# Kernel tuning notes

Hardware: AMD Instinct MI355X
Metric: run time of the kernel (lower is better)

## Reference

```python
import jax, jax.numpy as jnp
import numpy as np

B, S, D, H = 2, 2048, 2048, 16
HD = D // H  # 128
MAX_POS = 2048


def make_sinusoidal_positions(num_pos, dim):
    inv_freq = 1.0 / 10000 ** (np.arange(0, dim, 2) / dim)
    freqs = np.einsum('i,j->ij', np.arange(num_pos), inv_freq).astype('float32')
    emb = np.concatenate((freqs, freqs), axis=-1)  # (num_pos, dim)
    out = np.concatenate((np.sin(emb)[:, None, :], np.cos(emb)[:, None, :]), axis=-1)  # (num_pos,1,2*dim)
    return jnp.array(out[:, :, :num_pos])  # slice is a no-op since num_pos >= 2*dim


_SINCOS = make_sinusoidal_positions(MAX_POS, HD)


def rotate_half(x):
    return jnp.concatenate((-x[..., x.shape[-1] // 2:], x[..., :x.shape[-1] // 2]), axis=-1)


def setup_inputs() -> dict:
    key = jax.random.key(0)
    ks = jax.random.split(key, 5)
    std = 0.02
    return {
        'hidden_states': jax.random.normal(ks[0], (B, S, D), jnp.float32),
        'attention_mask': jnp.ones((B, S), jnp.int32),
        'position_ids': jnp.broadcast_to(jnp.arange(S, dtype=jnp.int32), (B, S)),
        'Wq': jax.random.normal(ks[1], (D, D), jnp.float32) * std,
        'Wk': jax.random.normal(ks[2], (D, D), jnp.float32) * std,
        'Wv': jax.random.normal(ks[3], (D, D), jnp.float32) * std,
        'Wo': jax.random.normal(ks[4], (D, D), jnp.float32) * std,
    }


def reference(hidden_states, attention_mask, position_ids, Wq, Wk, Wv, Wo):
    b, s, d = hidden_states.shape
    # QKV projections, split heads -> (b, s, H, HD)
    q = (hidden_states @ Wq).reshape(b, s, H, HD)
    k = (hidden_states @ Wk).reshape(b, s, H, HD)
    v = (hidden_states @ Wv).reshape(b, s, H, HD)
    # RoPE: embed_positions[position_ids] -> (b, s, 1, 2*HD); split -> sin, cos (b,s,1,HD)
    sincos = _SINCOS[position_ids]
    sin_pos, cos_pos = jnp.split(sincos, 2, axis=-1)
    q = q * cos_pos + rotate_half(q) * sin_pos
    k = k * cos_pos + rotate_half(k) * sin_pos
    # causal + padding mask -> additive bias
    causal = jnp.tril(jnp.ones((s, s), dtype=bool))  # (q, k)
    mask = (attention_mask[:, None, None, :] > 0) & causal[None, None, :, :]  # (b,1,s,s)
    bias = jnp.where(mask, jnp.float32(0.0), jnp.finfo(q.dtype).min).astype(q.dtype)
    # dot_product_attention_weights: scale query, scores + bias, softmax
    scale = jnp.asarray(1.0 / np.sqrt(HD), q.dtype)
    scores = jnp.einsum('bqhd,bkhd->bhqk', q * scale, k) + bias
    attn = jax.nn.softmax(scores, axis=-1)
    out = jnp.einsum('bhqk,bkhd->bqhd', attn, v).reshape(b, s, d)
    return out @ Wo
```

## Files before the change

kernel.cpp:

```cpp
#include <hip/hip_runtime.h>
#include <stdint.h>
#include <math.h>

#define BATCH 2
#define SEQ 2048
#define DM 2048
#define NH 16
#define HD 128

typedef unsigned short u16;
typedef __attribute__((ext_vector_type(8))) __bf16 bf16x8;
typedef __attribute__((ext_vector_type(8))) _Float16 f16x8;
typedef __attribute__((ext_vector_type(4))) float f32x4;
typedef __attribute__((ext_vector_type(4))) unsigned short u16x4;

__device__ inline float bf2f(u16 x) {
    return __uint_as_float(((unsigned)x) << 16);
}
__device__ inline u16 f2bf(float f) {
    unsigned u = __float_as_uint(f);
    return (u16)((u + 0x7FFF + ((u >> 16) & 1)) >> 16);
}
__device__ inline u16 f2h(float f) {
    union { _Float16 h; u16 u; } c;
    c.h = (_Float16)f;
    return c.u;
}
__device__ inline f32x4 mfma16(bf16x8 a, bf16x8 b, f32x4 c) {
    return __builtin_amdgcn_mfma_f32_16x16x32_bf16(a, b, c, 0, 0, 0);
}
__device__ inline f32x4 mfma16h(f16x8 a, f16x8 b, f32x4 c) {
    return __builtin_amdgcn_mfma_f32_16x16x32_f16(a, b, c, 0, 0, 0);
}
__device__ inline void cp16(const u16* g, u16* l) {
    __builtin_amdgcn_global_load_lds(
        (const __attribute__((address_space(1))) unsigned int*)g,
        (__attribute__((address_space(3))) unsigned int*)l, 16, 0, 0);
}

__global__ __launch_bounds__(256) void transpose4(const float* __restrict__ s0,
                                                  const float* __restrict__ s1,
                                                  const float* __restrict__ s2,
                                                  const float* __restrict__ s3,
                                                  u16* __restrict__ d0,
                                                  u16* __restrict__ d1,
                                                  u16* __restrict__ d2,
                                                  u16* __restrict__ d3) {
    __shared__ u16 tile[32][33];
    const float* src; u16* dst;
    switch (blockIdx.z) {
        case 0: src = s0; dst = d0; break;
        case 1: src = s1; dst = d1; break;
        case 2: src = s2; dst = d2; break;
        default: src = s3; dst = d3; break;
    }
    int bx = blockIdx.x * 32, by = blockIdx.y * 32;
    int tx = threadIdx.x & 31, ty = threadIdx.x >> 5;
    #pragma unroll
    for (int i = 0; i < 32; i += 8)
        tile[ty + i][tx] = f2bf(src[(long)(by + ty + i) * DM + bx + tx]);
    __syncthreads();
    #pragma unroll
    for (int i = 0; i < 32; i += 8)
        dst[(long)(bx + ty + i) * DM + by + tx] = tile[tx][ty + i];
}

__global__ __launch_bounds__(256) void xcast(const float* __restrict__ X,
                                             u16* __restrict__ Xb) {
    long i = ((long)blockIdx.x * 256 + threadIdx.x) * 8;
    float4 v0 = *(const float4*)&X[i];
    float4 v1 = *(const float4*)&X[i + 4];
    union { uint4 q; u16 e[8]; } u;
    u.e[0] = f2bf(v0.x); u.e[1] = f2bf(v0.y);
    u.e[2] = f2bf(v0.z); u.e[3] = f2bf(v0.w);
    u.e[4] = f2bf(v1.x); u.e[5] = f2bf(v1.y);
    u.e[6] = f2bf(v1.z); u.e[7] = f2bf(v1.w);
    *(uint4*)&Xb[i] = u.q;
}

#define BM 128
#define BN 128
#define BK 64

__global__ __launch_bounds__(256) void gemm_qkv(const u16* __restrict__ A,
                                                const u16* __restrict__ Wcat,
                                                u16* __restrict__ Qb,
                                                u16* __restrict__ Kb,
                                                u16* __restrict__ Vt) {
    __shared__ alignas(16) u16 As[BM * BK];
    __shared__ alignas(16) u16 Bs[BN * BK];
    int tid = threadIdx.x;
    int wave = tid >> 6, lane = tid & 63;
    int quad = lane >> 4, l16 = lane & 15;
    int wm = wave & 1, wn = wave >> 1;
    long rowBase = (long)blockIdx.y * BM;
    long colG = (long)blockIdx.x * BN;
    int mat = (int)(colG >> 11);
    long colBase = colG & (DM - 1);

    f32x4 acc[4][4];
    #pragma unroll
    for (int i = 0; i < 4; i++)
        #pragma unroll
        for (int j = 0; j < 4; j++) acc[i][j] = (f32x4){0.f, 0.f, 0.f, 0.f};

    for (int k0 = 0; k0 < DM; k0 += BK) {
        #pragma unroll
        for (int p = 0; p < 4; p++) {
            int idx = (p << 8) + tid;
            int r = idx >> 3, c8 = (idx & 7) << 3;
            cp16(&A[(rowBase + r) * DM + k0 + c8], &As[idx << 3]);
            cp16(&Wcat[(colG + r) * DM + k0 + c8], &Bs[idx << 3]);
        }
        __syncthreads();
        #pragma unroll
        for (int kk = 0; kk < 2; kk++) {
            bf16x8 af[4], bfr[4];
            #pragma unroll
            for (int i = 0; i < 4; i++)
                af[i] = *(const bf16x8*)&As[(wm * 64 + i * 16 + l16) * 64 + kk * 32 + quad * 8];
            #pragma unroll
            for (int j = 0; j < 4; j++)
                bfr[j] = *(const bf16x8*)&Bs[(wn * 64 + j * 16 + l16) * 64 + kk * 32 + quad * 8];
            #pragma unroll
            for (int i = 0; i < 4; i++)
                #pragma unroll
                for (int j = 0; j < 4; j++)
                    acc[i][j] = mfma16(af[i], bfr[j], acc[i][j]);
        }
        __syncthreads();
    }
    #pragma unroll
    for (int i = 0; i < 4; i++) {
        #pragma unroll
        for (int j = 0; j < 4; j++) {
            long col = colBase + wn * 64 + j * 16 + l16;
            if (mat == 2) {
                long row0 = rowBase + wm * 64 + i * 16 + quad * 4;
                long bb = row0 >> 11, ss = row0 & (SEQ - 1);
                long hh = col >> 7, dd = col & (HD - 1);
                u16x4 pk;
                #pragma unroll
                for (int r = 0; r < 4; r++) pk[r] = f2h(acc[i][j][r]);
                *(u16x4*)&Vt[(((bb * NH) + hh) * HD + dd) * SEQ + ss] = pk;
            } else {
                u16* C = (mat == 0) ? Qb : Kb;
                #pragma unroll
                for (int r = 0; r < 4; r++) {
                    long row = rowBase + wm * 64 + i * 16 + quad * 4 + r;
                    C[row * DM + col] = f2bf(acc[i][j][r]);
                }
            }
        }
    }
}

__global__ __launch_bounds__(256) void gemm_out(const u16* __restrict__ A,
                                                const u16* __restrict__ Bt,
                                                float* __restrict__ C) {
    __shared__ alignas(16) u16 As[BM * BK];
    __shared__ alignas(16) u16 Bs[BN * BK];
    int tid = threadIdx.x;
    int wave = tid >> 6, lane = tid & 63;
    int quad = lane >> 4, l16 = lane & 15;
    int wm = wave & 1, wn = wave >> 1;
    long rowBase = (long)blockIdx.y * BM;
    long colBase = (long)blockIdx.x * BN;

    f32x4 acc[4][4];
    #pragma unroll
    for (int i = 0; i < 4; i++)
        #pragma unroll
        for (int j = 0; j < 4; j++) acc[i][j] = (f32x4){0.f, 0.f, 0.f, 0.f};

    for (int k0 = 0; k0 < DM; k0 += BK) {
        #pragma unroll
        for (int p = 0; p < 4; p++) {
            int idx = (p << 8) + tid;
            int r = idx >> 3, c8 = (idx & 7) << 3;
            cp16(&A[(rowBase + r) * DM + k0 + c8], &As[idx << 3]);
            cp16(&Bt[(colBase + r) * DM + k0 + c8], &Bs[idx << 3]);
        }
        __syncthreads();
        #pragma unroll
        for (int kk = 0; kk < 2; kk++) {
            bf16x8 af[4], bfr[4];
            #pragma unroll
            for (int i = 0; i < 4; i++)
                af[i] = *(const bf16x8*)&As[(wm * 64 + i * 16 + l16) * 64 + kk * 32 + quad * 8];
            #pragma unroll
            for (int j = 0; j < 4; j++)
                bfr[j] = *(const bf16x8*)&Bs[(wn * 64 + j * 16 + l16) * 64 + kk * 32 + quad * 8];
            #pragma unroll
            for (int i = 0; i < 4; i++)
                #pragma unroll
                for (int j = 0; j < 4; j++)
                    acc[i][j] = mfma16(af[i], bfr[j], acc[i][j]);
        }
        __syncthreads();
    }
    #pragma unroll
    for (int i = 0; i < 4; i++)
        #pragma unroll
        for (int j = 0; j < 4; j++) {
            long col = colBase + wn * 64 + j * 16 + l16;
            #pragma unroll
            for (int r = 0; r < 4; r++) {
                long row = rowBase + wm * 64 + i * 16 + quad * 4 + r;
                C[row * DM + col] = acc[i][j][r];
            }
        }
}

__global__ __launch_bounds__(256) void rope_kernel(u16* __restrict__ Q,
                                                   u16* __restrict__ Kb,
                                                   const int* __restrict__ pid) {
    int idx = blockIdx.x * blockDim.x + threadIdx.x;
    int d = idx & 63;
    int h = (idx >> 6) & (NH - 1);
    int m = idx >> 10;
    int b = m >> 11, s = m & (SEQ - 1);
    int pos = pid[b * SEQ + s];
    float invf = __builtin_amdgcn_exp2f(-(float)d * 0.20762050593046015f);
    float freq = (float)pos * invf;
    float sn = __sinf(freq);
    float cs = __cosf(freq);
    long base = (long)m * DM + h * HD + d;
    float x1 = bf2f(Q[base]), x2 = bf2f(Q[base + 64]);
    Q[base] = f2bf(x1 * cs - x2 * sn);
    Q[base + 64] = f2bf(x2 * cs + x1 * sn);
    float y1 = bf2f(Kb[base]), y2 = bf2f(Kb[base + 64]);
    Kb[base] = f2bf(y1 * cs - y2 * sn);
    Kb[base + 64] = f2bf(y2 * cs + y1 * sn);
}

__global__ __launch_bounds__(128) void attn_mfma(const u16* __restrict__ Q,
                                                 const u16* __restrict__ K,
                                                 const u16* __restrict__ Vt,
                                                 const int* __restrict__ amask,
                                                 u16* __restrict__ O) {
    __shared__ alignas(16) char smem[19456];
    int tid = threadIdx.x;
    int w = tid >> 6, lane = tid & 63;
    int quad = lane >> 4, l16 = lane & 15;
    int bh = blockIdx.x;
    int qblk = gridDim.y - 1 - blockIdx.y;
    int b = bh >> 4, h = bh & (NH - 1);
    int qbase = qblk * 32;
    long head = (long)b * SEQ * DM + (long)h * HD;
    const u16* Vh = Vt + (long)bh * HD * SEQ;
    const int* mrow = amask + b * SEQ;
    u16* Pw = (u16*)smem + w * (32 * 72);

    bf16x8 qf[2][4];
    #pragma unroll
    for (int i = 0; i < 2; i++)
        #pragma unroll
        for (int kk = 0; kk < 4; kk++)
            qf[i][kk] = *(const bf16x8*)&Q[head + (long)(qbase + i * 16 + l16) * DM + kk * 32 + quad * 8];

    f32x4 of[2][8];
    #pragma unroll
    for (int i = 0; i < 2; i++)
        #pragma unroll
        for (int j = 0; j < 8; j++) of[i][j] = (f32x4){0.f, 0.f, 0.f, 0.f};
    float lsum[2][4] = {{0.f, 0.f, 0.f, 0.f}, {0.f, 0.f, 0.f, 0.f}};
    const float k2 = 0.12752792143808157f;
    const float C2 = 7.213475204444817f;

    int ntiles = (qbase + 32 + 63) >> 6;
    for (int t = w; t < ntiles; t += 2) {
        int kv0 = t << 6;
        bf16x8 kf[16];
        #pragma unroll
        for (int half = 0; half < 4; half++)
            #pragma unroll
            for (int kk = 0; kk < 4; kk++)
                kf[half * 4 + kk] = *(const bf16x8*)&K[head + (long)(kv0 + half * 16 + l16) * DM + kk * 32 + quad * 8];
        int am[4];
        #pragma unroll
        for (int half = 0; half < 4; half++) am[half] = mrow[kv0 + half * 16 + l16];
        f32x4 sacc[2][4];
        #pragma unroll
        for (int i = 0; i < 2; i++)
            #pragma unroll
            for (int half = 0; half < 4; half++) sacc[i][half] = (f32x4){0.f, 0.f, 0.f, 0.f};
        #pragma unroll
        for (int half = 0; half < 4; half++)
            #pragma unroll
            for (int kk = 0; kk < 4; kk++) {
                sacc[0][half] = mfma16(qf[0][kk], kf[half * 4 + kk], sacc[0][half]);
                sacc[1][half] = mfma16(qf[1][kk], kf[half * 4 + kk], sacc[1][half]);
            }
        #pragma unroll
        for (int i = 0; i < 2; i++)
            #pragma unroll
            for (int half = 0; half < 4; half++) {
                int kvc = kv0 + half * 16 + l16;
                #pragma unroll
                for (int r = 0; r < 4; r++) {
                    int qr = qbase + i * 16 + quad * 4 + r;
                    float p = (kvc <= qr && am[half] > 0)
                                  ? __builtin_amdgcn_exp2f(sacc[i][half][r] * k2 - C2) : 0.f;
                    lsum[i][r] += p;
                    Pw[(i * 16 + quad * 4 + r) * 72 + half * 16 + l16] = f2h(p);
                }
            }
        f16x8 pf[2][2];
        #pragma unroll
        for (int i = 0; i < 2; i++)
            #pragma unroll
            for (int c = 0; c < 2; c++)
                pf[i][c] = *(const f16x8*)&Pw[(i * 16 + l16) * 72 + c * 32 + quad * 8];
        #pragma unroll
        for (int c = 0; c < 2; c++)
            #pragma unroll
            for (int j = 0; j < 8; j++) {
                f16x8 vf = *(const f16x8*)&Vh[(long)(j * 16 + l16) * SEQ + kv0 + c * 32 + quad * 8];
                of[0][j] = mfma16h(pf[0][c], vf, of[0][j]);
                of[1][j] = mfma16h(pf[1][c], vf, of[1][j]);
            }
    }
    __syncthreads();
    float* of_lds = (float*)smem;
    float* ls_lds = (float*)(smem + 17408);
    if (w == 1) {
        #pragma unroll
        for (int i = 0; i < 2; i++)
            #pragma unroll
            for (int j = 0; j < 8; j++)
                *(f32x4*)&of_lds[lane * 68 + (i * 8 + j) * 4] = of[i][j];
        #pragma unroll
        for (int i = 0; i < 2; i++)
            #pragma unroll
            for (int r = 0; r < 4; r++) ls_lds[lane * 8 + i * 4 + r] = lsum[i][r];
    }
    __syncthreads();
    if (w == 0) {
        #pragma unroll
        for (int i = 0; i < 2; i++)
            #pragma unroll
            for (int j = 0; j < 8; j++) {
                f32x4 v = *(const f32x4*)&of_lds[lane * 68 + (i * 8 + j) * 4];
                of[i][j] += v;
            }
        #pragma unroll
        for (int i = 0; i < 2; i++)
            #pragma unroll
            for (int r = 0; r < 4; r++) lsum[i][r] += ls_lds[lane * 8 + i * 4 + r];
        #pragma unroll
        for (int i = 0; i < 2; i++) {
            float inv[4];
            #pragma unroll
            for (int r = 0; r < 4; r++) {
                float s = lsum[i][r];
                s += __shfl_xor(s, 1, 64);
                s += __shfl_xor(s, 2, 64);
                s += __shfl_xor(s, 4, 64);
                s += __shfl_xor(s, 8, 64);
                inv[r] = 1.0f / s;
            }
            #pragma unroll
            for (int j = 0; j < 8; j++)
                #pragma unroll
                for (int r = 0; r < 4; r++)
                    O[head + (long)(qbase + i * 16 + quad * 4 + r) * DM + j * 16 + l16] =
                        f2bf(of[i][j][r] * inv[r]);
        }
    }
}

extern "C" void kernel_launch(void* const* d_in, const int* in_sizes, int n_in,
                              void* d_out, int out_size, void* d_ws, size_t ws_size,
                              hipStream_t stream) {
    const float* X  = (const float*)d_in[0];
    const int* am   = (const int*)d_in[1];
    const int* pid  = (const int*)d_in[2];
    const float* Wq = (const float*)d_in[3];
    const float* Wk = (const float*)d_in[4];
    const float* Wv = (const float*)d_in[5];
    const float* Wo = (const float*)d_in[6];
    float* out = (float*)d_out;

    char* ws = (char*)d_ws;
    const size_t MB = 1024 * 1024;
    u16* WoT = (u16*)(ws + 0 * MB);
    u16* WqT = (u16*)(ws + 8 * MB);
    u16* WkT = (u16*)(ws + 16 * MB);
    u16* WvT = (u16*)(ws + 24 * MB);
    u16* Qb  = (u16*)(ws + 32 * MB);
    u16* Kb  = (u16*)(ws + 48 * MB);
    u16* Xb  = (u16*)d_out;
    u16* Vt  = (u16*)((char*)d_out + 16 * MB);

    dim3 tb(256);
    transpose4<<<dim3(64, 64, 4), tb, 0, stream>>>(Wq, Wk, Wv, Wo, WqT, WkT, WvT, WoT);
    xcast<<<(BATCH * SEQ * DM) / (256 * 8), tb, 0, stream>>>(X, Xb);

    gemm_qkv<<<dim3(3 * DM / BN, (BATCH * SEQ) / BM), tb, 0, stream>>>(Xb, WqT, Qb, Kb, Vt);

    int nrope = BATCH * SEQ * NH * 64;
    rope_kernel<<<nrope / 256, tb, 0, stream>>>(Qb, Kb, pid);

    dim3 ag(BATCH * NH, SEQ / 32);
    attn_mfma<<<ag, dim3(128), 0, stream>>>(Qb, Kb, Vt, am, Qb);

    gemm_out<<<dim3(DM / BN, (BATCH * SEQ) / BM), tb, 0, stream>>>(Qb, WoT, out);
}
```

Measured before the change: 478.1 us.

## Double-buffer GEMM LDS tiles with XOR swizzle and raise wave priority around MFMAs

Both projection GEMMs now share a macro that double-buffers the A and B tiles in LDS, issuing async copies for the next K-tile while the current one is multiplied. This drops one barrier per iteration. The LDS layout is XOR-swizzled by row to avoid bank conflicts on the 16-byte fragment reads. In the attention kernel, s_setprio brackets the QK and PV MFMA blocks so those waves get issue priority. The GEMM change doubles LDS use per block to 64KB, which may reduce occupancy.

```diff
diff --git a/kernel.cpp b/kernel.cpp
--- a/kernel.cpp
+++ b/kernel.cpp
@@ -82,54 +82,73 @@
 #define BN 128
 #define BK 64
 
+#define GEMM_PRE(Aptr, aR0, Bptr, bR0, Kdim)                                  \
+    __shared__ alignas(16) u16 As[2][BM * BK];                                \
+    __shared__ alignas(16) u16 Bs[2][BM * BK];                                \
+    int tid = threadIdx.x;                                                    \
+    int lane = tid & 63;                                                      \
+    int quad = lane >> 4, l16 = lane & 15;                                    \
+    int wm = (tid >> 6) & 1, wn = tid >> 7;                                   \
+    const u16* aSrc[4];                                                       \
+    const u16* bSrc[4];                                                       \
+    int ldst[4];                                                              \
+    for (int p = 0; p < 4; p++) {                                             \
+        int idx = (p << 8) + tid;                                             \
+        int r = idx >> 3, sl = idx & 7;                                       \
+        int sc = (sl ^ (r & 7)) << 3;                                         \
+        aSrc[p] = &(Aptr)[((aR0) + r) * (Kdim) + sc];                         \
+        bSrc[p] = &(Bptr)[((bR0) + r) * (Kdim) + sc];                         \
+        ldst[p] = idx << 3;                                                   \
+    }                                                                         \
+    f32x4 acc[4][4];                                                          \
+    for (int i = 0; i < 4; i++)                                               \
+        for (int j = 0; j < 4; j++) acc[i][j] = (f32x4){0.f, 0.f, 0.f, 0.f};  \
+    for (int p = 0; p < 4; p++) {                                             \
+        cp16(aSrc[p], &As[0][ldst[p]]);                                       \
+        cp16(bSrc[p], &Bs[0][ldst[p]]);                                       \
+        aSrc[p] += BK; bSrc[p] += BK;                                         \
+    }                                                                         \
+    __syncthreads();                                                          \
+    int NT = (Kdim) / BK;                                                     \
+    int cur = 0;                                                              \
+    for (int t = 0; t < NT; ++t) {                                            \
+        if (t + 1 < NT) {                                                     \
+            for (int p = 0; p < 4; p++) {                                     \
+                cp16(aSrc[p], &As[cur ^ 1][ldst[p]]);                         \
+                cp16(bSrc[p], &Bs[cur ^ 1][ldst[p]]);                         \
+                aSrc[p] += BK; bSrc[p] += BK;                                 \
+            }                                                                 \
+        }                                                                     \
+        _Pragma("unroll")                                                     \
+        for (int kk = 0; kk < 2; kk++) {                                      \
+            int sA = ((kk * 4 + quad) ^ (l16 & 7)) << 3;                      \
+            bf16x8 af[4], bfr[4];                                             \
+            _Pragma("unroll")                                                 \
+            for (int i = 0; i < 4; i++)                                       \
+                af[i] = *(const bf16x8*)&As[cur][(wm * 64 + i * 16 + l16) * 64 + sA]; \
+            _Pragma("unroll")                                                 \
+            for (int j = 0; j < 4; j++)                                       \
+                bfr[j] = *(const bf16x8*)&Bs[cur][(wn * 64 + j * 16 + l16) * 64 + sA]; \
+            _Pragma("unroll")                                                 \
+            for (int i = 0; i < 4; i++)                                       \
+                _Pragma("unroll")                                             \
+                for (int j = 0; j < 4; j++)                                   \
+                    acc[i][j] = mfma16(af[i], bfr[j], acc[i][j]);             \
+        }                                                                     \
+        __syncthreads();                                                      \
+        cur ^= 1;                                                             \
+    }
+
 __global__ __launch_bounds__(256) void gemm_qkv(const u16* __restrict__ A,
                                                 const u16* __restrict__ Wcat,
                                                 u16* __restrict__ Qb,
                                                 u16* __restrict__ Kb,
                                                 u16* __restrict__ Vt) {
-    __shared__ alignas(16) u16 As[BM * BK];
-    __shared__ alignas(16) u16 Bs[BN * BK];
-    int tid = threadIdx.x;
-    int wave = tid >> 6, lane = tid & 63;
-    int quad = lane >> 4, l16 = lane & 15;
-    int wm = wave & 1, wn = wave >> 1;
     long rowBase = (long)blockIdx.y * BM;
     long colG = (long)blockIdx.x * BN;
     int mat = (int)(colG >> 11);
     long colBase = colG & (DM - 1);
-
-    f32x4 acc[4][4];
-    #pragma unroll
-    for (int i = 0; i < 4; i++)
-        #pragma unroll
-        for (int j = 0; j < 4; j++) acc[i][j] = (f32x4){0.f, 0.f, 0.f, 0.f};
-
-    for (int k0 = 0; k0 < DM; k0 += BK) {
-        #pragma unroll
-        for (int p = 0; p < 4; p++) {
-            int idx = (p << 8) + tid;
-            int r = idx >> 3, c8 = (idx & 7) << 3;
-            cp16(&A[(rowBase + r) * DM + k0 + c8], &As[idx << 3]);
-            cp16(&Wcat[(colG + r) * DM + k0 + c8], &Bs[idx << 3]);
-        }
-        __syncthreads();
-        #pragma unroll
-        for (int kk = 0; kk < 2; kk++) {
-            bf16x8 af[4], bfr[4];
-            #pragma unroll
-            for (int i = 0; i < 4; i++)
-                af[i] = *(const bf16x8*)&As[(wm * 64 + i * 16 + l16) * 64 + kk * 32 + quad * 8];
-            #pragma unroll
-            for (int j = 0; j < 4; j++)
-                bfr[j] = *(const bf16x8*)&Bs[(wn * 64 + j * 16 + l16) * 64 + kk * 32 + quad * 8];
-            #pragma unroll
-            for (int i = 0; i < 4; i++)
-                #pragma unroll
-                for (int j = 0; j < 4; j++)
-                    acc[i][j] = mfma16(af[i], bfr[j], acc[i][j]);
-        }
-        __syncthreads();
-    }
+    GEMM_PRE(A, rowBase, Wcat, colG, DM)
     #pragma unroll
     for (int i = 0; i < 4; i++) {
         #pragma unroll
@@ -158,47 +177,9 @@
 __global__ __launch_bounds__(256) void gemm_out(const u16* __restrict__ A,
                                                 const u16* __restrict__ Bt,
                                                 float* __restrict__ C) {
-    __shared__ alignas(16) u16 As[BM * BK];
-    __shared__ alignas(16) u16 Bs[BN * BK];
-    int tid = threadIdx.x;
-    int wave = tid >> 6, lane = tid & 63;
-    int quad = lane >> 4, l16 = lane & 15;
-    int wm = wave & 1, wn = wave >> 1;
     long rowBase = (long)blockIdx.y * BM;
     long colBase = (long)blockIdx.x * BN;
-
-    f32x4 acc[4][4];
-    #pragma unroll
-    for (int i = 0; i < 4; i++)
-        #pragma unroll
-        for (int j = 0; j < 4; j++) acc[i][j] = (f32x4){0.f, 0.f, 0.f, 0.f};
-
-    for (int k0 = 0; k0 < DM; k0 += BK) {
-        #pragma unroll
-        for (int p = 0; p < 4; p++) {
-            int idx = (p << 8) + tid;
-            int r = idx >> 3, c8 = (idx & 7) << 3;
-            cp16(&A[(rowBase + r) * DM + k0 + c8], &As[idx << 3]);
-            cp16(&Bt[(colBase + r) * DM + k0 + c8], &Bs[idx << 3]);
-        }
-        __syncthreads();
-        #pragma unroll
-        for (int kk = 0; kk < 2; kk++) {
-            bf16x8 af[4], bfr[4];
-            #pragma unroll
-            for (int i = 0; i < 4; i++)
-                af[i] = *(const bf16x8*)&As[(wm * 64 + i * 16 + l16) * 64 + kk * 32 + quad * 8];
-            #pragma unroll
-            for (int j = 0; j < 4; j++)
-                bfr[j] = *(const bf16x8*)&Bs[(wn * 64 + j * 16 + l16) * 64 + kk * 32 + quad * 8];
-            #pragma unroll
-            for (int i = 0; i < 4; i++)
-                #pragma unroll
-                for (int j = 0; j < 4; j++)
-                    acc[i][j] = mfma16(af[i], bfr[j], acc[i][j]);
-        }
-        __syncthreads();
-    }
+    GEMM_PRE(A, rowBase, Bt, colBase, DM)
     #pragma unroll
     for (int i = 0; i < 4; i++)
         #pragma unroll
@@ -285,6 +266,7 @@
         for (int i = 0; i < 2; i++)
             #pragma unroll
             for (int half = 0; half < 4; half++) sacc[i][half] = (f32x4){0.f, 0.f, 0.f, 0.f};
+        __builtin_amdgcn_s_setprio(1);
         #pragma unroll
         for (int half = 0; half < 4; half++)
             #pragma unroll
@@ -292,6 +274,7 @@
                 sacc[0][half] = mfma16(qf[0][kk], kf[half * 4 + kk], sacc[0][half]);
                 sacc[1][half] = mfma16(qf[1][kk], kf[half * 4 + kk], sacc[1][half]);
             }
+        __builtin_amdgcn_s_setprio(0);
         #pragma unroll
         for (int i = 0; i < 2; i++)
             #pragma unroll
@@ -312,6 +295,7 @@
             #pragma unroll
             for (int c = 0; c < 2; c++)
                 pf[i][c] = *(const f16x8*)&Pw[(i * 16 + l16) * 72 + c * 32 + quad * 8];
+        __builtin_amdgcn_s_setprio(1);
         #pragma unroll
         for (int c = 0; c < 2; c++)
             #pragma unroll
@@ -320,6 +304,7 @@
                 of[0][j] = mfma16h(pf[0][c], vf, of[0][j]);
                 of[1][j] = mfma16h(pf[1][c], vf, of[1][j]);
             }
+        __builtin_amdgcn_s_setprio(0);
     }
     __syncthreads();
     float* of_lds = (float*)smem;
```

New measurement: 445.5 us. 1.07x faster.
